# Kernel optimization log

Hardware: AMD Instinct MI355X
Metric: run time of the kernel (lower is better)

Reference implementation:

```python
import jax, jax.numpy as jnp
import numpy as np

SEQ, B, XD = 2048, 4, 16
D, NH, DFF, L, M = 256, 8, 512, 2, 1024
DH = D // NH
NEG_INF = -1e9  # finite stand-in for -inf (same softmax result, grad-safe)


def setup_inputs() -> dict:
    key = jax.random.key(0)
    ks = iter(jax.random.split(key, 40))

    def w(shape, s=0.02):
        return jax.random.normal(next(ks), shape, dtype=jnp.float32) * s

    return {
        "x": jax.random.normal(next(ks), (SEQ, B, XD), dtype=jnp.float32),
        "y": jax.random.normal(next(ks), (SEQ, B), dtype=jnp.float32),
        "single_eval_pos": M,
        "xenc_w": w((D, XD)), "xenc_b": w((D,)),
        "yenc_w": w((D, 1)), "yenc_b": w((D,)),
        "in_proj_w": w((L, 3 * D, D)), "in_proj_b": w((L, 3 * D)),
        "out_proj_w": w((L, D, D)), "out_proj_b": w((L, D)),
        "ln1_g": jnp.ones((L, D), jnp.float32), "ln1_b": jnp.zeros((L, D), jnp.float32),
        "lin1_w": w((L, DFF, D)), "lin1_b": w((L, DFF)),
        "lin2_w": w((L, D, DFF)), "lin2_b": w((L, D)),
        "ln2_g": jnp.ones((L, D), jnp.float32), "ln2_b": jnp.zeros((L, D), jnp.float32),
        "head_w1": w((DFF, D)), "head_b1": w((DFF,)),
        "head_w2": w((1, DFF)), "head_b2": w((1,)),
    }


def _layer_norm(x, g, b, eps=1e-5):
    mu = jnp.mean(x, axis=-1, keepdims=True)
    var = jnp.var(x, axis=-1, keepdims=True)
    return (x - mu) * jax.lax.rsqrt(var + eps) * g + b


def _forward(x, y, M_, p):
    seq, batch = y.shape
    x_src = x @ p["xenc_w"].T + p["xenc_b"]                     # [seq, b, D]
    y_src = y[..., None] @ p["yenc_w"].T + p["yenc_b"]           # [seq, b, D]
    tokens = jnp.concatenate([x_src[:M_] + y_src[:M_], x_src[M_:]], axis=0)

    # prefix-block + diagonal mask: keep (j < M) or (i == j)
    i = jnp.arange(seq)
    keep = (i[None, :] < M_) | (i[:, None] == i[None, :])
    mask = jnp.where(keep, 0.0, NEG_INF).astype(tokens.dtype)    # [seq, seq]

    h = tokens
    for l in range(p["in_proj_w"].shape[0]):
        qkv = h @ p["in_proj_w"][l].T + p["in_proj_b"][l]        # [seq, b, 3D]
        q, k, v = jnp.split(qkv, 3, axis=-1)
        to_heads = lambda t: t.reshape(seq, batch, NH, DH).transpose(1, 2, 0, 3)
        q, k, v = to_heads(q), to_heads(k), to_heads(v)          # [b, h, s, dh]
        scores = jnp.einsum("bhqd,bhkd->bhqk", q, k) / np.float32(np.sqrt(DH)) + mask
        attn = jax.nn.softmax(scores, axis=-1)
        o = jnp.einsum("bhqk,bhkd->bhqd", attn, v)
        o = o.transpose(2, 0, 1, 3).reshape(seq, batch, D)
        o = o @ p["out_proj_w"][l].T + p["out_proj_b"][l]
        h = _layer_norm(h + o, p["ln1_g"][l], p["ln1_b"][l])      # post-norm
        ff = jax.nn.gelu(h @ p["lin1_w"][l].T + p["lin1_b"][l], approximate=False)
        ff = ff @ p["lin2_w"][l].T + p["lin2_b"][l]
        h = _layer_norm(h + ff, p["ln2_g"][l], p["ln2_b"][l])

    q_out = h[M_:]                                               # [seq-M, b, D]
    hid = jax.nn.gelu(q_out @ p["head_w1"].T + p["head_b1"], approximate=False)
    return hid @ p["head_w2"].T + p["head_b2"]                   # [seq-M, b, 1]


def reference(x, y, single_eval_pos, xenc_w, xenc_b, yenc_w, yenc_b,
              in_proj_w, in_proj_b, out_proj_w, out_proj_b,
              ln1_g, ln1_b, lin1_w, lin1_b, lin2_w, lin2_b, ln2_g, ln2_b,
              head_w1, head_b1, head_w2, head_b2):
    p = dict(xenc_w=xenc_w, xenc_b=xenc_b, yenc_w=yenc_w, yenc_b=yenc_b,
             in_proj_w=in_proj_w, in_proj_b=in_proj_b,
             out_proj_w=out_proj_w, out_proj_b=out_proj_b,
             ln1_g=ln1_g, ln1_b=ln1_b, lin1_w=lin1_w, lin1_b=lin1_b,
             lin2_w=lin2_w, lin2_b=lin2_b, ln2_g=ln2_g, ln2_b=ln2_b,
             head_w1=head_w1, head_b1=head_b1, head_w2=head_w2, head_b2=head_b2)
    return _forward(x, y, int(single_eval_pos), p)
```

## Files before the change

### kernel.cpp

```cpp
#include <hip/hip_runtime.h>
#include <hip/hip_bf16.h>
#include <math.h>

#define SEQ    2048
#define BATCH  4
#define XDIM   16
#define DMODEL 256
#define NHEAD  8
#define DH     32
#define DFF    512
#define NLAYER 2
#define MPOS   1024
#define ROWS   (SEQ*BATCH)

#define ATT_SCALE 0.17677669529663687f

typedef __attribute__((ext_vector_type(8))) short bf16x8;
typedef __attribute__((ext_vector_type(4))) float f32x4;

__device__ __forceinline__ float gelu_exact(float x) {
    return 0.5f * x * (1.0f + erff(x * 0.70710678118654752f));
}
__device__ __forceinline__ short f2bf(float f) {
    unsigned int u = __float_as_uint(f);
    u += 0x7FFFu + ((u >> 16) & 1u);
    return (short)(u >> 16);
}
__device__ __forceinline__ float bf2f(unsigned short u) {
    return __uint_as_float(((unsigned int)u) << 16);
}
__device__ __forceinline__ void gload16(const unsigned short* g, unsigned short* l) {
    __builtin_amdgcn_global_load_lds(
        (const __attribute__((address_space(1))) unsigned int*)g,
        (__attribute__((address_space(3))) unsigned int*)l, 16, 0, 0);
}
#define VMWAIT(N) asm volatile("s_waitcnt vmcnt(" #N ")" ::: "memory")
__device__ __forceinline__ void pipe_barrier() {
    __builtin_amdgcn_sched_barrier(0);
    __builtin_amdgcn_s_barrier();
    __builtin_amdgcn_sched_barrier(0);
}

__global__ __launch_bounds__(256) void encode_cast(
    const float* __restrict__ x, const float* __restrict__ y,
    const float* __restrict__ xw, const float* __restrict__ xb,
    const float* __restrict__ yw, const float* __restrict__ yb,
    float* __restrict__ h, unsigned short* __restrict__ hb,
    const float* __restrict__ s0, const float* __restrict__ s1,
    const float* __restrict__ s2, const float* __restrict__ s3,
    const float* __restrict__ s4,
    unsigned short* __restrict__ d0, unsigned short* __restrict__ d1,
    unsigned short* __restrict__ d2, unsigned short* __restrict__ d3,
    unsigned short* __restrict__ d4)
{
    if (blockIdx.x < ROWS/4) {
        int g = blockIdx.x;
        int d = threadIdx.x;
        __shared__ float xs[4][XDIM];
        __shared__ float ys[4];
        if (d < 64) xs[d>>4][d&15] = x[(size_t)(g*4 + (d>>4))*XDIM + (d&15)];
        if (d < 4)  ys[d] = y[g*4 + d];
        __syncthreads();
        float wreg[XDIM];
        #pragma unroll
        for (int k = 0; k < XDIM; ++k) wreg[k] = xw[d*XDIM + k];
        const float xbv = xb[d], ywv = yw[d], ybv = yb[d];
        const bool train = (g < MPOS);
        #pragma unroll
        for (int r = 0; r < 4; ++r) {
            int row = g*4 + r;
            float acc = xbv;
            #pragma unroll
            for (int k = 0; k < XDIM; ++k) acc = fmaf(xs[r][k], wreg[k], acc);
            if (train) acc += ys[r]*ywv + ybv;
            h[(size_t)row*DMODEL + d]  = acc;
            hb[(size_t)row*DMODEL + d] = (unsigned short)f2bf(acc);
        }
        return;
    }
    int i = (blockIdx.x - ROWS/4)*256 + threadIdx.x;
    if (i >= 147456) return;
    const float* s; unsigned short* d; int off;
    if      (i <  49152) { s = s0; d = d0; off = i; }
    else if (i <  65536) { s = s1; d = d1; off = i - 49152; }
    else if (i <  98304) { s = s2; d = d2; off = i - 65536; }
    else if (i < 131072) { s = s3; d = d3; off = i - 98304; }
    else                 { s = s4; d = d4; off = i - 131072; }
    float4 a = *(const float4*)(s + (size_t)off*8);
    float4 c = *(const float4*)(s + (size_t)off*8 + 4);
    ushort4 u0, u1;
    u0.x=(unsigned short)f2bf(a.x); u0.y=(unsigned short)f2bf(a.y);
    u0.z=(unsigned short)f2bf(a.z); u0.w=(unsigned short)f2bf(a.w);
    u1.x=(unsigned short)f2bf(c.x); u1.y=(unsigned short)f2bf(c.y);
    u1.z=(unsigned short)f2bf(c.z); u1.w=(unsigned short)f2bf(c.w);
    *(ushort4*)(d + (size_t)off*8)     = u0;
    *(ushort4*)(d + (size_t)off*8 + 4) = u1;
}

__global__ __launch_bounds__(256) void gemm_qkv(
    const unsigned short* __restrict__ A, const unsigned short* __restrict__ B,
    const float* __restrict__ bias,
    unsigned short* __restrict__ Qg, unsigned short* __restrict__ Kg,
    unsigned short* __restrict__ Vg, int K)
{
    __shared__ unsigned short As[2][128][64];
    __shared__ unsigned short Bs[2][64][64];
    int tid  = threadIdx.x;
    int w    = tid >> 6, lane = tid & 63;
    int col  = lane & 15, quad = lane >> 4;
    int u    = blockIdx.x >> 3, xcd = blockIdx.x & 7;
    int by   = xcd*8 + u/12, bx = u%12;
    int m0   = by * 128, n0 = bx * 64;
    int l8   = lane >> 3;
    int c8s  = (((lane & 7) ^ l8) * 8);

    f32x4 acc[2][4];
    #pragma unroll
    for (int i = 0; i < 2; ++i)
        #pragma unroll
        for (int j = 0; j < 4; ++j) acc[i][j] = (f32x4){0.f,0.f,0.f,0.f};

    const unsigned short* ga = A + (size_t)(m0 + w*32 + l8)*K + c8s;
    const unsigned short* gb = B + (size_t)(n0 + w*16 + l8)*K + c8s;
    const int NS = K / 64;

    #pragma unroll
    for (int t = 0; t < 4; ++t) gload16(ga + (size_t)(t*8)*K, &As[0][w*32 + t*8][0]);
    #pragma unroll
    for (int t = 0; t < 2; ++t) gload16(gb + (size_t)(t*8)*K, &Bs[0][w*16 + t*8][0]);

    for (int s = 0; s < NS; ++s) {
        VMWAIT(0);
        pipe_barrier();
        if (s + 1 < NS) {
            int k2 = (s + 1) * 64;
            int nb = (s + 1) & 1;
            #pragma unroll
            for (int t = 0; t < 4; ++t) gload16(ga + k2 + (size_t)(t*8)*K, &As[nb][w*32 + t*8][0]);
            #pragma unroll
            for (int t = 0; t < 2; ++t) gload16(gb + k2 + (size_t)(t*8)*K, &Bs[nb][w*16 + t*8][0]);
        }
        int cur = s & 1;
        #pragma unroll
        for (int kk = 0; kk < 2; ++kk) {
            const int so = (((kk*4 + quad) ^ (col & 7)) * 8);
            bf16x8 af[2], bfr[4];
            #pragma unroll
            for (int i = 0; i < 2; ++i) af[i]  = *(const bf16x8*)&As[cur][w*32 + i*16 + col][so];
            #pragma unroll
            for (int j = 0; j < 4; ++j) bfr[j] = *(const bf16x8*)&Bs[cur][j*16 + col][so];
            #pragma unroll
            for (int i = 0; i < 2; ++i)
                #pragma unroll
                for (int j = 0; j < 4; ++j)
                    acc[i][j] = __builtin_amdgcn_mfma_f32_16x16x32_bf16(bfr[j], af[i], acc[i][j], 0, 0, 0);
        }
    }

    int region = n0 >> 8;
    if (region < 2) {
        #pragma unroll
        for (int i = 0; i < 2; ++i) {
            int m = m0 + w*32 + i*16 + col;
            int s = m >> 2, bidx = m & 3;
            #pragma unroll
            for (int j = 0; j < 4; ++j) {
                int ng = n0 + j*16 + quad*4;
                float4 bi = *(const float4*)&bias[ng];
                ushort4 uu;
                uu.x=(unsigned short)f2bf(acc[i][j][0] + bi.x);
                uu.y=(unsigned short)f2bf(acc[i][j][1] + bi.y);
                uu.z=(unsigned short)f2bf(acc[i][j][2] + bi.z);
                uu.w=(unsigned short)f2bf(acc[i][j][3] + bi.w);
                int np = ng - (region << 8);
                int hh = np >> 5, d = np & 31;
                int bh = bidx*NHEAD + hh;
                if (region == 0)
                    *(ushort4*)(Qg + ((size_t)(bh*SEQ + s))*DH + d) = uu;
                else
                    *(ushort4*)(Kg + ((size_t)(bh*SEQ + s))*DH + d) = uu;
            }
        }
    } else {
        __syncthreads();
        unsigned short* T3 = (unsigned short*)As;
        #pragma unroll
        for (int i = 0; i < 2; ++i) {
            int mi = w*32 + i*16 + col;
            int ss = mi >> 2, bidx = mi & 3;
            #pragma unroll
            for (int j = 0; j < 4; ++j) {
                int ni = j*16 + quad*4;
                float4 bi = *(const float4*)&bias[n0 + ni];
                T3[((ni    )*4 + bidx)*32 + ss] = (unsigned short)f2bf(acc[i][j][0] + bi.x);
                T3[((ni + 1)*4 + bidx)*32 + ss] = (unsigned short)f2bf(acc[i][j][1] + bi.y);
                T3[((ni + 2)*4 + bidx)*32 + ss] = (unsigned short)f2bf(acc[i][j][2] + bi.z);
                T3[((ni + 3)*4 + bidx)*32 + ss] = (unsigned short)f2bf(acc[i][j][3] + bi.w);
            }
        }
        __syncthreads();
        int sBase = m0 >> 2;
        #pragma unroll
        for (int r = 0; r < 4; ++r) {
            int chunk = tid + 256*r;
            int l = chunk >> 2, p = chunk & 3;
            int d = l & 31, hh_l = (l >> 5) & 1, bidx = l >> 6;
            int ni = hh_l*32 + d;
            int hh = ((n0 & 255) + ni) >> 5;
            int bh = bidx*NHEAD + hh;
            uint4 val = *(const uint4*)&T3[(ni*4 + bidx)*32 + p*8];
            *(uint4*)(Vg + ((size_t)(bh*DH + d))*SEQ + sBase + p*8) = val;
        }
    }
}

__global__ __launch_bounds__(256) void attn_mfma(
    const unsigned short* __restrict__ Qg,
    const unsigned short* __restrict__ Kg,
    const unsigned short* __restrict__ Vg,
    unsigned short* __restrict__ o)
{
    const int id  = blockIdx.x;
    const int sl  = id >> 3;
    const int bh  = (id & 7) * 4 + (sl >> 4);
    const int qt2 = sl & 15;
    const int h   = bh & 7;
    const int b   = bh >> 3;
    const int q0A = qt2 * 64;
    const int q0B = MPOS + qt2 * 64;
    const int tid  = threadIdx.x;
    const int w    = tid >> 6;
    const int lane = tid & 63;
    const int col  = lane & 15;
    const int quad = lane >> 4;

    __shared__ unsigned short Kt[2][128][40];
    __shared__ unsigned short Vt[2][32][136];
    __shared__ unsigned short PtA[4][16][136];
    __shared__ unsigned short PtB[4][16][136];

    const int qA = q0A + 16*w + col;
    const int qB = q0B + 16*w + col;
    bf16x8 qfA = *(const bf16x8*)(Qg + ((size_t)(bh*SEQ + qA))*DH + quad*8);
    bf16x8 qfB = *(const bf16x8*)(Qg + ((size_t)(bh*SEQ + qB))*DH + quad*8);

    f32x4 O0A = {0.f,0.f,0.f,0.f}, O1A = {0.f,0.f,0.f,0.f};
    f32x4 O0B = {0.f,0.f,0.f,0.f}, O1B = {0.f,0.f,0.f,0.f};
    float lsumA = 0.f, lsumB = 0.f;

    const int kRow = tid >> 2, kCh = (tid & 3) * 8;
    const int vD   = tid >> 3, vCh = (tid & 7) * 8;

    uint4 kreg0 = *(const uint4*)(Kg + ((size_t)(bh*SEQ + kRow     ))*DH + kCh);
    uint4 kreg1 = *(const uint4*)(Kg + ((size_t)(bh*SEQ + kRow + 64))*DH + kCh);
    uint4 vreg0 = *(const uint4*)(Vg + ((size_t)(bh*DH + vD))*SEQ + vCh);
    uint4 vreg1 = *(const uint4*)(Vg + ((size_t)(bh*DH + vD))*SEQ + vCh + 64);

    for (int kt = 0; kt < 8; ++kt) {
        const int p = kt & 1;
        *(uint4*)&Kt[p][kRow     ][kCh] = kreg0;
        *(uint4*)&Kt[p][kRow + 64][kCh] = kreg1;
        *(uint4*)&Vt[p][vD][vCh     ]   = vreg0;
        *(uint4*)&Vt[p][vD][vCh + 64]   = vreg1;
        __syncthreads();
        if (kt < 7) {
            int kn = (kt + 1) * 128;
            kreg0 = *(const uint4*)(Kg + ((size_t)(bh*SEQ + kn + kRow     ))*DH + kCh);
            kreg1 = *(const uint4*)(Kg + ((size_t)(bh*SEQ + kn + kRow + 64))*DH + kCh);
            vreg0 = *(const uint4*)(Vg + ((size_t)(bh*DH + vD))*SEQ + kn + vCh);
            vreg1 = *(const uint4*)(Vg + ((size_t)(bh*DH + vD))*SEQ + kn + vCh + 64);
        } else {
            kreg0 = *(const uint4*)(Kg + ((size_t)(bh*SEQ + q0B + kRow))*DH + kCh);
            vreg0 = *(const uint4*)(Vg + ((size_t)(bh*DH + vD))*SEQ + q0B + vCh);
        }

        #pragma unroll
        for (int mt = 0; mt < 8; ++mt) {
            bf16x8 kf = *(const bf16x8*)&Kt[p][mt*16 + col][quad*8];
            f32x4 stA = {0.f,0.f,0.f,0.f};
            stA = __builtin_amdgcn_mfma_f32_16x16x32_bf16(kf, qfA, stA, 0, 0, 0);
            ushort4 pwA;
            #pragma unroll
            for (int i = 0; i < 4; ++i) {
                float pv = __expf(stA[i]*ATT_SCALE);
                unsigned short us = (unsigned short)f2bf(pv);
                ((unsigned short*)&pwA)[i] = us;
                lsumA += bf2f(us);
            }
            *(ushort4*)&PtA[w][col][mt*16 + quad*4] = pwA;

            f32x4 stB = {0.f,0.f,0.f,0.f};
            stB = __builtin_amdgcn_mfma_f32_16x16x32_bf16(kf, qfB, stB, 0, 0, 0);
            ushort4 pwB;
            #pragma unroll
            for (int i = 0; i < 4; ++i) {
                float pv = __expf(stB[i]*ATT_SCALE);
                unsigned short us = (unsigned short)f2bf(pv);
                ((unsigned short*)&pwB)[i] = us;
                lsumB += bf2f(us);
            }
            *(ushort4*)&PtB[w][col][mt*16 + quad*4] = pwB;
        }
        #pragma unroll
        for (int c = 0; c < 4; ++c) {
            bf16x8 v0 = *(const bf16x8*)&Vt[p][col     ][c*32 + quad*8];
            bf16x8 v1 = *(const bf16x8*)&Vt[p][col + 16][c*32 + quad*8];
            bf16x8 pfA = *(const bf16x8*)&PtA[w][col][c*32 + quad*8];
            O0A = __builtin_amdgcn_mfma_f32_16x16x32_bf16(v0, pfA, O0A, 0, 0, 0);
            O1A = __builtin_amdgcn_mfma_f32_16x16x32_bf16(v1, pfA, O1A, 0, 0, 0);
            bf16x8 pfB = *(const bf16x8*)&PtB[w][col][c*32 + quad*8];
            O0B = __builtin_amdgcn_mfma_f32_16x16x32_bf16(v0, pfB, O0B, 0, 0, 0);
            O1B = __builtin_amdgcn_mfma_f32_16x16x32_bf16(v1, pfB, O1B, 0, 0, 0);
        }
    }

    *(uint4*)&Kt[0][kRow][kCh] = kreg0;
    *(uint4*)&Vt[0][vD][vCh]   = vreg0;
    __syncthreads();
    #pragma unroll
    for (int mt = 0; mt < 4; ++mt) {
        bf16x8 kf = *(const bf16x8*)&Kt[0][mt*16 + col][quad*8];
        f32x4 stB = {0.f,0.f,0.f,0.f};
        stB = __builtin_amdgcn_mfma_f32_16x16x32_bf16(kf, qfB, stB, 0, 0, 0);
        ushort4 pwB;
        #pragma unroll
        for (int i = 0; i < 4; ++i) {
            float pv = __expf(stB[i]*ATT_SCALE);
            if (mt*16 + quad*4 + i != 16*w + col) pv = 0.f;
            unsigned short us = (unsigned short)f2bf(pv);
            ((unsigned short*)&pwB)[i] = us;
            lsumB += bf2f(us);
        }
        *(ushort4*)&PtB[w][col][mt*16 + quad*4] = pwB;
    }
    #pragma unroll
    for (int c = 0; c < 2; ++c) {
        bf16x8 v0 = *(const bf16x8*)&Vt[0][col     ][c*32 + quad*8];
        bf16x8 v1 = *(const bf16x8*)&Vt[0][col + 16][c*32 + quad*8];
        bf16x8 pfB = *(const bf16x8*)&PtB[w][col][c*32 + quad*8];
        O0B = __builtin_amdgcn_mfma_f32_16x16x32_bf16(v0, pfB, O0B, 0, 0, 0);
        O1B = __builtin_amdgcn_mfma_f32_16x16x32_bf16(v1, pfB, O1B, 0, 0, 0);
    }

    lsumA += __shfl_xor(lsumA, 16, 64); lsumA += __shfl_xor(lsumA, 32, 64);
    lsumB += __shfl_xor(lsumB, 16, 64); lsumB += __shfl_xor(lsumB, 32, 64);
    float invA = 1.0f / lsumA, invB = 1.0f / lsumB;
    ushort4 u0, u1;
    #pragma unroll
    for (int i = 0; i < 4; ++i) {
        ((unsigned short*)&u0)[i] = (unsigned short)f2bf(O0A[i]*invA);
        ((unsigned short*)&u1)[i] = (unsigned short)f2bf(O1A[i]*invA);
    }
    unsigned short* opA = o + ((size_t)(qA*BATCH + b))*DMODEL + h*DH;
    *(ushort4*)(opA + quad*4)      = u0;
    *(ushort4*)(opA + 16 + quad*4) = u1;
    #pragma unroll
    for (int i = 0; i < 4; ++i) {
        ((unsigned short*)&u0)[i] = (unsigned short)f2bf(O0B[i]*invB);
        ((unsigned short*)&u1)[i] = (unsigned short)f2bf(O1B[i]*invB);
    }
    unsigned short* opB = o + ((size_t)(qB*BATCH + b))*DMODEL + h*DH;
    *(ushort4*)(opB + quad*4)      = u0;
    *(ushort4*)(opB + 16 + quad*4) = u1;
}

__global__ __launch_bounds__(512) void mlp_fused(
    const unsigned short* __restrict__ attb,
    const unsigned short* __restrict__ Wout, const float* __restrict__ ob,
    const float* __restrict__ g1, const float* __restrict__ be1,
    const unsigned short* __restrict__ W1, const float* __restrict__ fb1,
    const unsigned short* __restrict__ W2, const float* __restrict__ fb2,
    const float* __restrict__ g2, const float* __restrict__ be2,
    float* __restrict__ h, unsigned short* __restrict__ hb,
    const unsigned short* __restrict__ Wh1, const float* __restrict__ hb1,
    const float* __restrict__ hw2, const float* __restrict__ hb2,
    float* __restrict__ out, int doHead)
{
    __shared__ unsigned short Bs[3][256][64];
    __shared__ __align__(16) unsigned char smem_u[33280];
    __shared__ unsigned short Ht[2][16][264];
    __shared__ float sP[2][8][16], qP[2][8][16];

    typedef unsigned short AsT[2][16][64];
    AsT* As = reinterpret_cast<AsT*>(smem_u);
    typedef unsigned short PtT[16][520];
    PtT* Pt = reinterpret_cast<PtT*>(smem_u);

    const int tid  = threadIdx.x;
    const int w    = tid >> 6;
    const int lane = tid & 63;
    const int col  = lane & 15;
    const int quad = lane >> 4;
    const int l8   = lane >> 3;
    const int c8s  = (((lane & 7) ^ l8) * 8);
    const int bid  = blockIdx.x;
    const int m0a  = bid * 16;
    const int m0b  = 4096 + bid * 16;
    const int ma   = m0a + col;
    const int mb   = m0b + col;

    float resid[2][2][4];

    {
        f32x4 acc[2][2];
        #pragma unroll
        for (int g = 0; g < 2; ++g)
            #pragma unroll
            for (int j = 0; j < 2; ++j) acc[g][j] = (f32x4){0.f,0.f,0.f,0.f};

        const int gr = w >> 1;
        const unsigned short* gaw = attb + (size_t)((gr ? m0b : m0a) + (w&1)*8 + l8)*DMODEL + c8s;
        const unsigned short* gb  = Wout + (size_t)(w*32 + l8)*DMODEL + c8s;
        const int NS = DMODEL / 64;

        #pragma unroll
        for (int pb = 0; pb < 2; ++pb) {
            int k = pb * 64;
            if (w < 4) gload16(gaw + k, &As[pb][gr][(w&1)*8][0]);
            #pragma unroll
            for (int t = 0; t < 4; ++t)
                gload16(gb + k + (size_t)(t*8)*DMODEL, &Bs[pb][w*32 + t*8][0]);
        }
        int bcur = 0;
        for (int s = 0; s < NS; ++s) {
            if (s == NS - 1)      { VMWAIT(0); }
            else if (w < 4)       { VMWAIT(5); }
            else                  { VMWAIT(4); }
            pipe_barrier();
            if (s + 2 < NS) {
                int bpre = bcur + 2; if (bpre >= 3) bpre -= 3;
                int k2 = (s + 2) * 64;
                if (w < 4) gload16(gaw + k2, &As[bpre][gr][(w&1)*8][0]);
                #pragma unroll
                for (int t = 0; t < 4; ++t)
                    gload16(gb + k2 + (size_t)(t*8)*DMODEL, &Bs[bpre][w*32 + t*8][0]);
            }
            #pragma unroll
            for (int kk = 0; kk < 2; ++kk) {
                const int so = (((kk*4 + quad) ^ (col & 7)) * 8);
                bf16x8 af0 = *(const bf16x8*)&As[bcur][0][col][so];
                bf16x8 af1 = *(const bf16x8*)&As[bcur][1][col][so];
                #pragma unroll
                for (int j = 0; j < 2; ++j) {
                    bf16x8 bfr = *(const bf16x8*)&Bs[bcur][w*32 + j*16 + col][so];
                    acc[0][j] = __builtin_amdgcn_mfma_f32_16x16x32_bf16(bfr, af0, acc[0][j], 0, 0, 0);
                    acc[1][j] = __builtin_amdgcn_mfma_f32_16x16x32_bf16(bfr, af1, acc[1][j], 0, 0, 0);
                }
            }
            bcur = (bcur == 2) ? 0 : bcur + 1;
        }

        float ssum[2] = {0.f, 0.f}, qsum[2] = {0.f, 0.f};
        #pragma unroll
        for (int g = 0; g < 2; ++g) {
            int m = g ? mb : ma;
            #pragma unroll
            for (int j = 0; j < 2; ++j) {
                int n = w*32 + j*16 + quad*4;
                float4 bi = *(const float4*)&ob[n];
                float4 hv = *(const float4*)&h[(size_t)m*DMODEL + n];
                #pragma unroll
                for (int i = 0; i < 4; ++i) {
                    float val = acc[g][j][i] + ((const float*)&bi)[i] + ((const float*)&hv)[i];
                    resid[g][j][i] = val;
                    ssum[g] += val; qsum[g] += val*val;
                }
            }
        }
        #pragma unroll
        for (int g = 0; g < 2; ++g) {
            ssum[g] += __shfl_xor(ssum[g], 16, 64); ssum[g] += __shfl_xor(ssum[g], 32, 64);
            qsum[g] += __shfl_xor(qsum[g], 16, 64); qsum[g] += __shfl_xor(qsum[g], 32, 64);
        }
        if (quad == 0) {
            sP[0][w][col] = ssum[0]; qP[0][w][col] = qsum[0];
            sP[1][w][col] = ssum[1]; qP[1][w][col] = qsum[1];
        }
        __syncthreads();
        #pragma unroll
        for (int g = 0; g < 2; ++g) {
            float st = 0.f, qt = 0.f;
            #pragma unroll
            for (int ww = 0; ww < 8; ++ww) { st += sP[g][ww][col]; qt += qP[g][ww][col]; }
            float mu   = st * (1.0f/DMODEL);
            float var  = qt * (1.0f/DMODEL) - mu*mu;
            float rstd = rsqrtf(var + 1e-5f);
            #pragma unroll
            for (int j = 0; j < 2; ++j) {
                int n = w*32 + j*16 + quad*4;
                float4 gv = *(const float4*)&g1[n];
                float4 bv = *(const float4*)&be1[n];
                ushort4 u;
                #pragma unroll
                for (int i = 0; i < 4; ++i) {
                    float o = (resid[g][j][i]-mu)*rstd*((const float*)&gv)[i] + ((const float*)&bv)[i];
                    resid[g][j][i] = o;
                    ((unsigned short*)&u)[i] = (unsigned short)f2bf(o);
                }
                *(ushort4*)&Ht[g][col][n] = u;
            }
        }
        __syncthreads();
    }

    #pragma unroll 1
    for (int nh = 0; nh < 2; ++nh) {
        f32x4 acc[2][2];
        #pragma unroll
        for (int g = 0; g < 2; ++g)
            #pragma unroll
            for (int j = 0; j < 2; ++j) acc[g][j] = (f32x4){0.f,0.f,0.f,0.f};
        const unsigned short* gb = W1 + (size_t)(nh*256 + w*32 + l8)*DMODEL + c8s;
        const int NS = DMODEL / 64;

        #pragma unroll
        for (int pb = 0; pb < 2; ++pb)
            #pragma unroll
            for (int t = 0; t < 4; ++t)
                gload16(gb + pb*64 + (size_t)(t*8)*DMODEL, &Bs[pb][w*32 + t*8][0]);

        int bcur = 0;
        for (int s = 0; s < NS; ++s) {
            if (s == NS - 1) { VMWAIT(0); } else { VMWAIT(4); }
            pipe_barrier();
            if (s + 2 < NS) {
                int bpre = bcur + 2; if (bpre >= 3) bpre -= 3;
                int k2 = (s + 2) * 64;
                #pragma unroll
                for (int t = 0; t < 4; ++t)
                    gload16(gb + k2 + (size_t)(t*8)*DMODEL, &Bs[bpre][w*32 + t*8][0]);
            }
            #pragma unroll
            for (int kk = 0; kk < 2; ++kk) {
                const int so = (((kk*4 + quad) ^ (col & 7)) * 8);
                bf16x8 af0 = *(const bf16x8*)&Ht[0][col][s*64 + kk*32 + quad*8];
                bf16x8 af1 = *(const bf16x8*)&Ht[1][col][s*64 + kk*32 + quad*8];
                #pragma unroll
                for (int j = 0; j < 2; ++j) {
                    bf16x8 bfr = *(const bf16x8*)&Bs[bcur][w*32 + j*16 + col][so];
                    acc[0][j] = __builtin_amdgcn_mfma_f32_16x16x32_bf16(bfr, af0, acc[0][j], 0, 0, 0);
                    acc[1][j] = __builtin_amdgcn_mfma_f32_16x16x32_bf16(bfr, af1, acc[1][j], 0, 0, 0);
                }
            }
            bcur = (bcur == 2) ? 0 : bcur + 1;
        }
        #pragma unroll
        for (int g = 0; g < 2; ++g)
            #pragma unroll
            for (int j = 0; j < 2; ++j) {
                int n2 = nh*256 + w*32 + j*16 + quad*4;
                float4 bi = *(const float4*)&fb1[n2];
                ushort4 u;
                #pragma unroll
                for (int i = 0; i < 4; ++i)
                    ((unsigned short*)&u)[i] = (unsigned short)f2bf(gelu_exact(acc[g][j][i] + ((const float*)&bi)[i]));
                *(ushort4*)&Pt[g][col][n2] = u;
            }
        pipe_barrier();
    }

    {
        __syncthreads();
        f32x4 acc[2][2];
        #pragma unroll
        for (int g = 0; g < 2; ++g)
            #pragma unroll
            for (int j = 0; j < 2; ++j) acc[g][j] = (f32x4){0.f,0.f,0.f,0.f};
        const unsigned short* gb = W2 + (size_t)(w*32 + l8)*DFF + c8s;
        const int NS = DFF / 64;

        #pragma unroll
        for (int pb = 0; pb < 2; ++pb)
            #pragma unroll
            for (int t = 0; t < 4; ++t)
                gload16(gb + pb*64 + (size_t)(t*8)*DFF, &Bs[pb][w*32 + t*8][0]);

        int bcur = 0;
        for (int s = 0; s < NS; ++s) {
            if (s == NS - 1) { VMWAIT(0); } else { VMWAIT(4); }
            pipe_barrier();
            if (s + 2 < NS) {
                int bpre = bcur + 2; if (bpre >= 3) bpre -= 3;
                int k2 = (s + 2) * 64;
                #pragma unroll
                for (int t = 0; t < 4; ++t)
                    gload16(gb + k2 + (size_t)(t*8)*DFF, &Bs[bpre][w*32 + t*8][0]);
            }
            #pragma unroll
            for (int kk = 0; kk < 2; ++kk) {
                const int so = (((kk*4 + quad) ^ (col & 7)) * 8);
                bf16x8 af0 = *(const bf16x8*)&Pt[0][col][s*64 + kk*32 + quad*8];
                bf16x8 af1 = *(const bf16x8*)&Pt[1][col][s*64 + kk*32 + quad*8];
                #pragma unroll
                for (int j = 0; j < 2; ++j) {
                    bf16x8 bfr = *(const bf16x8*)&Bs[bcur][w*32 + j*16 + col][so];
                    acc[0][j] = __builtin_amdgcn_mfma_f32_16x16x32_bf16(bfr, af0, acc[0][j], 0, 0, 0);
                    acc[1][j] = __builtin_amdgcn_mfma_f32_16x16x32_bf16(bfr, af1, acc[1][j], 0, 0, 0);
                }
            }
            bcur = (bcur == 2) ? 0 : bcur + 1;
        }

        float ssum[2] = {0.f, 0.f}, qsum[2] = {0.f, 0.f};
        #pragma unroll
        for (int g = 0; g < 2; ++g)
            #pragma unroll
            for (int j = 0; j < 2; ++j) {
                int n = w*32 + j*16 + quad*4;
                float4 bi = *(const float4*)&fb2[n];
                #pragma unroll
                for (int i = 0; i < 4; ++i) {
                    float val = acc[g][j][i] + ((const float*)&bi)[i] + resid[g][j][i];
                    resid[g][j][i] = val;
                    ssum[g] += val; qsum[g] += val*val;
                }
            }
        #pragma unroll
        for (int g = 0; g < 2; ++g) {
            ssum[g] += __shfl_xor(ssum[g], 16, 64); ssum[g] += __shfl_xor(ssum[g], 32, 64);
            qsum[g] += __shfl_xor(qsum[g], 16, 64); qsum[g] += __shfl_xor(qsum[g], 32, 64);
        }
        if (quad == 0) {
            sP[0][w][col] = ssum[0]; qP[0][w][col] = qsum[0];
            sP[1][w][col] = ssum[1]; qP[1][w][col] = qsum[1];
        }
        __syncthreads();
        #pragma unroll
        for (int g = 0; g < 2; ++g) {
            int m = g ? mb : ma;
            float st = 0.f, qt = 0.f;
            #pragma unroll
            for (int ww = 0; ww < 8; ++ww) { st += sP[g][ww][col]; qt += qP[g][ww][col]; }
            float mu   = st * (1.0f/DMODEL);
            float var  = qt * (1.0f/DMODEL) - mu*mu;
            float rstd = rsqrtf(var + 1e-5f);
            #pragma unroll
            for (int j = 0; j < 2; ++j) {
                int n = w*32 + j*16 + quad*4;
                float4 gv = *(const float4*)&g2[n];
                float4 bv = *(const float4*)&be2[n];
                float4 o;
                ushort4 u;
                #pragma unroll
                for (int i = 0; i < 4; ++i) {
                    float ov = (resid[g][j][i]-mu)*rstd*((const float*)&gv)[i] + ((const float*)&bv)[i];
                    ((float*)&o)[i] = ov;
                    ((unsigned short*)&u)[i] = (unsigned short)f2bf(ov);
                }
                *(float4*)&h[(size_t)m*DMODEL + n] = o;
                *(ushort4*)(hb + (size_t)m*DMODEL + n) = u;
                *(ushort4*)&Ht[g][col][n] = u;
            }
        }
        __syncthreads();
    }

    if (doHead) {
        float sdot = 0.f;
        #pragma unroll 1
        for (int nh = 0; nh < 2; ++nh) {
            f32x4 acc[2];
            #pragma unroll
            for (int j = 0; j < 2; ++j) acc[j] = (f32x4){0.f,0.f,0.f,0.f};
            const unsigned short* gb = Wh1 + (size_t)(nh*256 + w*32 + l8)*DMODEL + c8s;
            const int NS = DMODEL / 64;

            #pragma unroll
            for (int pb = 0; pb < 2; ++pb)
                #pragma unroll
                for (int t = 0; t < 4; ++t)
                    gload16(gb + pb*64 + (size_t)(t*8)*DMODEL, &Bs[pb][w*32 + t*8][0]);

            int bcur = 0;
            for (int s = 0; s < NS; ++s) {
                if (s == NS - 1) { VMWAIT(0); } else { VMWAIT(4); }
                pipe_barrier();
                if (s + 2 < NS) {
                    int bpre = bcur + 2; if (bpre >= 3) bpre -= 3;
                    int k2 = (s + 2) * 64;
                    #pragma unroll
                    for (int t = 0; t < 4; ++t)
                        gload16(gb + k2 + (size_t)(t*8)*DMODEL, &Bs[bpre][w*32 + t*8][0]);
                }
                #pragma unroll
                for (int kk = 0; kk < 2; ++kk) {
                    const int so = (((kk*4 + quad) ^ (col & 7)) * 8);
                    bf16x8 af = *(const bf16x8*)&Ht[1][col][s*64 + kk*32 + quad*8];
                    #pragma unroll
                    for (int j = 0; j < 2; ++j) {
                        bf16x8 bfr = *(const bf16x8*)&Bs[bcur][w*32 + j*16 + col][so];
                        acc[j] = __builtin_amdgcn_mfma_f32_16x16x32_bf16(bfr, af, acc[j], 0, 0, 0);
                    }
                }
                bcur = (bcur == 2) ? 0 : bcur + 1;
            }
            #pragma unroll
            for (int j = 0; j < 2; ++j) {
                int n2 = nh*256 + w*32 + j*16 + quad*4;
                float4 b1v = *(const float4*)&hb1[n2];
                float4 w2v = *(const float4*)&hw2[n2];
                #pragma unroll
                for (int i = 0; i < 4; ++i)
                    sdot += gelu_exact(acc[j][i] + ((const float*)&b1v)[i]) * ((const float*)&w2v)[i];
            }
            pipe_barrier();
        }
        sdot += __shfl_xor(sdot, 16, 64); sdot += __shfl_xor(sdot, 32, 64);
        if (quad == 0) sP[0][w][col] = sdot;
        __syncthreads();
        if (tid < 16) {
            float r = hb2[0];
            #pragma unroll
            for (int ww = 0; ww < 8; ++ww) r += sP[0][ww][tid];
            out[bid*16 + tid] = r;
        }
    }
}

extern "C" void kernel_launch(void* const* d_in, const int* in_sizes, int n_in,
                              void* d_out, int out_size, void* d_ws, size_t ws_size,
                              hipStream_t stream)
{
    const float* x        = (const float*)d_in[0];
    const float* y        = (const float*)d_in[1];
    const float* xenc_w   = (const float*)d_in[3];
    const float* xenc_b   = (const float*)d_in[4];
    const float* yenc_w   = (const float*)d_in[5];
    const float* yenc_b   = (const float*)d_in[6];
    const float* in_proj_w  = (const float*)d_in[7];
    const float* in_proj_b  = (const float*)d_in[8];
    const float* out_proj_w = (const float*)d_in[9];
    const float* out_proj_b = (const float*)d_in[10];
    const float* ln1_g    = (const float*)d_in[11];
    const float* ln1_b    = (const float*)d_in[12];
    const float* lin1_w   = (const float*)d_in[13];
    const float* lin1_b   = (const float*)d_in[14];
    const float* lin2_w   = (const float*)d_in[15];
    const float* lin2_b   = (const float*)d_in[16];
    const float* ln2_g    = (const float*)d_in[17];
    const float* ln2_b    = (const float*)d_in[18];
    const float* head_w1  = (const float*)d_in[19];
    const float* head_b1  = (const float*)d_in[20];
    const float* head_w2  = (const float*)d_in[21];
    const float* head_b2  = (const float*)d_in[22];
    float* out = (float*)d_out;

    float* ws  = (float*)d_ws;
    float* h    = ws;
    unsigned short* hb    = (unsigned short*)(h + (size_t)ROWS*DMODEL);
    unsigned short* attb  = hb    + (size_t)ROWS*DMODEL;
    unsigned short* Qg    = attb  + (size_t)ROWS*DMODEL;
    unsigned short* Kg    = Qg    + (size_t)BATCH*NHEAD*SEQ*DH;
    unsigned short* Vg    = Kg    + (size_t)BATCH*NHEAD*SEQ*DH;
    unsigned short* Wqkv  = Vg    + (size_t)BATCH*NHEAD*SEQ*DH;
    unsigned short* Wout  = Wqkv  + (size_t)NLAYER*3*DMODEL*DMODEL;
    unsigned short* Wl1   = Wout  + (size_t)NLAYER*DMODEL*DMODEL;
    unsigned short* Wl2   = Wl1   + (size_t)NLAYER*DFF*DMODEL;
    unsigned short* Wh1   = Wl2   + (size_t)NLAYER*DMODEL*DFF;

    encode_cast<<<ROWS/4 + 576, 256, 0, stream>>>(
        x, y, xenc_w, xenc_b, yenc_w, yenc_b, h, hb,
        in_proj_w, out_proj_w, lin1_w, lin2_w, head_w1,
        Wqkv, Wout, Wl1, Wl2, Wh1);

    for (int l = 0; l < NLAYER; ++l) {
        gemm_qkv<<<768, 256, 0, stream>>>(
            hb, Wqkv + (size_t)l*3*DMODEL*DMODEL, in_proj_b + l*3*DMODEL,
            Qg, Kg, Vg, DMODEL);
        attn_mfma<<<512, 256, 0, stream>>>(Qg, Kg, Vg, attb);
        mlp_fused<<<256, 512, 0, stream>>>(
            attb,
            Wout + (size_t)l*DMODEL*DMODEL, out_proj_b + l*DMODEL,
            ln1_g + l*DMODEL, ln1_b + l*DMODEL,
            Wl1 + (size_t)l*DFF*DMODEL, lin1_b + l*DFF,
            Wl2 + (size_t)l*DMODEL*DFF, lin2_b + l*DMODEL,
            ln2_g + l*DMODEL, ln2_b + l*DMODEL,
            h, hb,
            Wh1, head_b1, head_w2, head_b2,
            out, (l == NLAYER-1) ? 1 : 0);
    }
}
```

Before: 229.9 us.

## Split attention query groups across 8 waves instead of 4 per block

The attention kernel now launches 512 threads per block. Waves 0-3 handle the context query tile and waves 4-7 handle the matching test query tile, where before each of 4 waves processed both tiles. Each thread loads one K and one V chunk instead of two, and the tail diagonal step runs only in the second group. This halves per-wave register and serial MFMA/exp work and adds more waves for latency hiding. In exchange there are more threads per sync and the first group sits idle during the tail step.

Result: no change. 226.3 us (-1.6%).

```diff
diff --git a/kernel.cpp b/kernel.cpp
--- a/kernel.cpp
+++ b/kernel.cpp
@@ -214,7 +214,7 @@
     }
 }
 
-__global__ __launch_bounds__(256) void attn_mfma(
+__global__ __launch_bounds__(512) void attn_mfma(
     const unsigned short* __restrict__ Qg,
     const unsigned short* __restrict__ Kg,
     const unsigned short* __restrict__ Vg,
@@ -230,138 +230,113 @@
     const int q0B = MPOS + qt2 * 64;
     const int tid  = threadIdx.x;
     const int w    = tid >> 6;
+    const int ws   = w & 3;
+    const int grp  = w >> 2;
     const int lane = tid & 63;
     const int col  = lane & 15;
     const int quad = lane >> 4;
 
     __shared__ unsigned short Kt[2][128][40];
     __shared__ unsigned short Vt[2][32][136];
-    __shared__ unsigned short PtA[4][16][136];
-    __shared__ unsigned short PtB[4][16][136];
-
-    const int qA = q0A + 16*w + col;
-    const int qB = q0B + 16*w + col;
-    bf16x8 qfA = *(const bf16x8*)(Qg + ((size_t)(bh*SEQ + qA))*DH + quad*8);
-    bf16x8 qfB = *(const bf16x8*)(Qg + ((size_t)(bh*SEQ + qB))*DH + quad*8);
-
-    f32x4 O0A = {0.f,0.f,0.f,0.f}, O1A = {0.f,0.f,0.f,0.f};
-    f32x4 O0B = {0.f,0.f,0.f,0.f}, O1B = {0.f,0.f,0.f,0.f};
-    float lsumA = 0.f, lsumB = 0.f;
-
-    const int kRow = tid >> 2, kCh = (tid & 3) * 8;
-    const int vD   = tid >> 3, vCh = (tid & 7) * 8;
-
-    uint4 kreg0 = *(const uint4*)(Kg + ((size_t)(bh*SEQ + kRow     ))*DH + kCh);
-    uint4 kreg1 = *(const uint4*)(Kg + ((size_t)(bh*SEQ + kRow + 64))*DH + kCh);
-    uint4 vreg0 = *(const uint4*)(Vg + ((size_t)(bh*DH + vD))*SEQ + vCh);
-    uint4 vreg1 = *(const uint4*)(Vg + ((size_t)(bh*DH + vD))*SEQ + vCh + 64);
+    __shared__ unsigned short Pt[8][16][136];
+
+    const int q0 = grp ? q0B : q0A;
+    const int q  = q0 + 16*ws + col;
+    bf16x8 qf = *(const bf16x8*)(Qg + ((size_t)(bh*SEQ + q))*DH + quad*8);
+
+    f32x4 O0 = {0.f,0.f,0.f,0.f};
+    f32x4 O1 = {0.f,0.f,0.f,0.f};
+    float lsum = 0.f;
+
+    const int kRow = tid >> 2,  kCh = (tid & 3) * 8;
+    const int vD   = tid >> 4,  vCh = (tid & 15) * 8;
+
+    uint4 kreg = *(const uint4*)(Kg + ((size_t)(bh*SEQ + kRow))*DH + kCh);
+    uint4 vreg = *(const uint4*)(Vg + ((size_t)(bh*DH + vD))*SEQ + vCh);
 
     for (int kt = 0; kt < 8; ++kt) {
         const int p = kt & 1;
-        *(uint4*)&Kt[p][kRow     ][kCh] = kreg0;
-        *(uint4*)&Kt[p][kRow + 64][kCh] = kreg1;
-        *(uint4*)&Vt[p][vD][vCh     ]   = vreg0;
-        *(uint4*)&Vt[p][vD][vCh + 64]   = vreg1;
+        *(uint4*)&Kt[p][kRow][kCh] = kreg;
+        *(uint4*)&Vt[p][vD][vCh]   = vreg;
         __syncthreads();
         if (kt < 7) {
             int kn = (kt + 1) * 128;
-            kreg0 = *(const uint4*)(Kg + ((size_t)(bh*SEQ + kn + kRow     ))*DH + kCh);
-            kreg1 = *(const uint4*)(Kg + ((size_t)(bh*SEQ + kn + kRow + 64))*DH + kCh);
-            vreg0 = *(const uint4*)(Vg + ((size_t)(bh*DH + vD))*SEQ + kn + vCh);
-            vreg1 = *(const uint4*)(Vg + ((size_t)(bh*DH + vD))*SEQ + kn + vCh + 64);
+            kreg = *(const uint4*)(Kg + ((size_t)(bh*SEQ + kn + kRow))*DH + kCh);
+            vreg = *(const uint4*)(Vg + ((size_t)(bh*DH + vD))*SEQ + kn + vCh);
         } else {
-            kreg0 = *(const uint4*)(Kg + ((size_t)(bh*SEQ + q0B + kRow))*DH + kCh);
-            vreg0 = *(const uint4*)(Vg + ((size_t)(bh*DH + vD))*SEQ + q0B + vCh);
+            if (kRow < 64)
+                kreg = *(const uint4*)(Kg + ((size_t)(bh*SEQ + q0B + kRow))*DH + kCh);
+            if (vCh < 64)
+                vreg = *(const uint4*)(Vg + ((size_t)(bh*DH + vD))*SEQ + q0B + vCh);
         }
 
         #pragma unroll
         for (int mt = 0; mt < 8; ++mt) {
             bf16x8 kf = *(const bf16x8*)&Kt[p][mt*16 + col][quad*8];
-            f32x4 stA = {0.f,0.f,0.f,0.f};
-            stA = __builtin_amdgcn_mfma_f32_16x16x32_bf16(kf, qfA, stA, 0, 0, 0);
-            ushort4 pwA;
+            f32x4 st = {0.f,0.f,0.f,0.f};
+            st = __builtin_amdgcn_mfma_f32_16x16x32_bf16(kf, qf, st, 0, 0, 0);
+            ushort4 pw;
             #pragma unroll
             for (int i = 0; i < 4; ++i) {
-                float pv = __expf(stA[i]*ATT_SCALE);
+                float pv = __expf(st[i]*ATT_SCALE);
                 unsigned short us = (unsigned short)f2bf(pv);
-                ((unsigned short*)&pwA)[i] = us;
-                lsumA += bf2f(us);
-            }
-            *(ushort4*)&PtA[w][col][mt*16 + quad*4] = pwA;
-
-            f32x4 stB = {0.f,0.f,0.f,0.f};
-            stB = __builtin_amdgcn_mfma_f32_16x16x32_bf16(kf, qfB, stB, 0, 0, 0);
-            ushort4 pwB;
-            #pragma unroll
-            for (int i = 0; i < 4; ++i) {
-                float pv = __expf(stB[i]*ATT_SCALE);
-                unsigned short us = (unsigned short)f2bf(pv);
-                ((unsigned short*)&pwB)[i] = us;
-                lsumB += bf2f(us);
-            }
-            *(ushort4*)&PtB[w][col][mt*16 + quad*4] = pwB;
+                ((unsigned short*)&pw)[i] = us;
+                lsum += bf2f(us);
+            }
+            *(ushort4*)&Pt[w][col][mt*16 + quad*4] = pw;
         }
         #pragma unroll
         for (int c = 0; c < 4; ++c) {
             bf16x8 v0 = *(const bf16x8*)&Vt[p][col     ][c*32 + quad*8];
             bf16x8 v1 = *(const bf16x8*)&Vt[p][col + 16][c*32 + quad*8];
-            bf16x8 pfA = *(const bf16x8*)&PtA[w][col][c*32 + quad*8];
-            O0A = __builtin_amdgcn_mfma_f32_16x16x32_bf16(v0, pfA, O0A, 0, 0, 0);
-            O1A = __builtin_amdgcn_mfma_f32_16x16x32_bf16(v1, pfA, O1A, 0, 0, 0);
-            bf16x8 pfB = *(const bf16x8*)&PtB[w][col][c*32 + quad*8];
-            O0B = __builtin_amdgcn_mfma_f32_16x16x32_bf16(v0, pfB, O0B, 0, 0, 0);
-            O1B = __builtin_amdgcn_mfma_f32_16x16x32_bf16(v1, pfB, O1B, 0, 0, 0);
-        }
-    }
-
-    *(uint4*)&Kt[0][kRow][kCh] = kreg0;
-    *(uint4*)&Vt[0][vD][vCh]   = vreg0;
+            bf16x8 pf = *(const bf16x8*)&Pt[w][col][c*32 + quad*8];
+            O0 = __builtin_amdgcn_mfma_f32_16x16x32_bf16(v0, pf, O0, 0, 0, 0);
+            O1 = __builtin_amdgcn_mfma_f32_16x16x32_bf16(v1, pf, O1, 0, 0, 0);
+        }
+    }
+
+    if (kRow < 64) *(uint4*)&Kt[0][kRow][kCh] = kreg;
+    if (vCh < 64)  *(uint4*)&Vt[0][vD][vCh]   = vreg;
     __syncthreads();
-    #pragma unroll
-    for (int mt = 0; mt < 4; ++mt) {
-        bf16x8 kf = *(const bf16x8*)&Kt[0][mt*16 + col][quad*8];
-        f32x4 stB = {0.f,0.f,0.f,0.f};
-        stB = __builtin_amdgcn_mfma_f32_16x16x32_bf16(kf, qfB, stB, 0, 0, 0);
-        ushort4 pwB;
-        #pragma unroll
-        for (int i = 0; i < 4; ++i) {
-            float pv = __expf(stB[i]*ATT_SCALE);
-            if (mt*16 + quad*4 + i != 16*w + col) pv = 0.f;
-            unsigned short us = (unsigned short)f2bf(pv);
-            ((unsigned short*)&pwB)[i] = us;
-            lsumB += bf2f(us);
-        }
-        *(ushort4*)&PtB[w][col][mt*16 + quad*4] = pwB;
-    }
-    #pragma unroll
-    for (int c = 0; c < 2; ++c) {
-        bf16x8 v0 = *(const bf16x8*)&Vt[0][col     ][c*32 + quad*8];
-        bf16x8 v1 = *(const bf16x8*)&Vt[0][col + 16][c*32 + quad*8];
-        bf16x8 pfB = *(const bf16x8*)&PtB[w][col][c*32 + quad*8];
-        O0B = __builtin_amdgcn_mfma_f32_16x16x32_bf16(v0, pfB, O0B, 0, 0, 0);
-        O1B = __builtin_amdgcn_mfma_f32_16x16x32_bf16(v1, pfB, O1B, 0, 0, 0);
-    }
-
-    lsumA += __shfl_xor(lsumA, 16, 64); lsumA += __shfl_xor(lsumA, 32, 64);
-    lsumB += __shfl_xor(lsumB, 16, 64); lsumB += __shfl_xor(lsumB, 32, 64);
-    float invA = 1.0f / lsumA, invB = 1.0f / lsumB;
+    if (grp == 1) {
+        #pragma unroll
+        for (int mt = 0; mt < 4; ++mt) {
+            bf16x8 kf = *(const bf16x8*)&Kt[0][mt*16 + col][quad*8];
+            f32x4 st = {0.f,0.f,0.f,0.f};
+            st = __builtin_amdgcn_mfma_f32_16x16x32_bf16(kf, qf, st, 0, 0, 0);
+            ushort4 pw;
+            #pragma unroll
+            for (int i = 0; i < 4; ++i) {
+                float pv = __expf(st[i]*ATT_SCALE);
+                if (mt*16 + quad*4 + i != 16*ws + col) pv = 0.f;
+                unsigned short us = (unsigned short)f2bf(pv);
+                ((unsigned short*)&pw)[i] = us;
+                lsum += bf2f(us);
+            }
+            *(ushort4*)&Pt[w][col][mt*16 + quad*4] = pw;
+        }
+        #pragma unroll
+        for (int c = 0; c < 2; ++c) {
+            bf16x8 v0 = *(const bf16x8*)&Vt[0][col     ][c*32 + quad*8];
+            bf16x8 v1 = *(const bf16x8*)&Vt[0][col + 16][c*32 + quad*8];
+            bf16x8 pf = *(const bf16x8*)&Pt[w][col][c*32 + quad*8];
+            O0 = __builtin_amdgcn_mfma_f32_16x16x32_bf16(v0, pf, O0, 0, 0, 0);
+            O1 = __builtin_amdgcn_mfma_f32_16x16x32_bf16(v1, pf, O1, 0, 0, 0);
+        }
+    }
+
+    lsum += __shfl_xor(lsum, 16, 64);
+    lsum += __shfl_xor(lsum, 32, 64);
+    float inv = 1.0f / lsum;
     ushort4 u0, u1;
     #pragma unroll
     for (int i = 0; i < 4; ++i) {
-        ((unsigned short*)&u0)[i] = (unsigned short)f2bf(O0A[i]*invA);
-        ((unsigned short*)&u1)[i] = (unsigned short)f2bf(O1A[i]*invA);
-    }
-    unsigned short* opA = o + ((size_t)(qA*BATCH + b))*DMODEL + h*DH;
-    *(ushort4*)(opA + quad*4)      = u0;
-    *(ushort4*)(opA + 16 + quad*4) = u1;
-    #pragma unroll
-    for (int i = 0; i < 4; ++i) {
-        ((unsigned short*)&u0)[i] = (unsigned short)f2bf(O0B[i]*invB);
-        ((unsigned short*)&u1)[i] = (unsigned short)f2bf(O1B[i]*invB);
-    }
-    unsigned short* opB = o + ((size_t)(qB*BATCH + b))*DMODEL + h*DH;
-    *(ushort4*)(opB + quad*4)      = u0;
-    *(ushort4*)(opB + 16 + quad*4) = u1;
+        ((unsigned short*)&u0)[i] = (unsigned short)f2bf(O0[i]*inv);
+        ((unsigned short*)&u1)[i] = (unsigned short)f2bf(O1[i]*inv);
+    }
+    unsigned short* op = o + ((size_t)(q*BATCH + b))*DMODEL + h*DH;
+    *(ushort4*)(op + quad*4)      = u0;
+    *(ushort4*)(op + 16 + quad*4) = u1;
 }
 
 __global__ __launch_bounds__(512) void mlp_fused(
@@ -767,7 +742,7 @@
         gemm_qkv<<<768, 256, 0, stream>>>(
             hb, Wqkv + (size_t)l*3*DMODEL*DMODEL, in_proj_b + l*3*DMODEL,
             Qg, Kg, Vg, DMODEL);
-        attn_mfma<<<512, 256, 0, stream>>>(Qg, Kg, Vg, attb);
+        attn_mfma<<<512, 512, 0, stream>>>(Qg, Kg, Vg, attb);
         mlp_fused<<<256, 512, 0, stream>>>(
             attb,
             Wout + (size_t)l*DMODEL*DMODEL, out_proj_b + l*DMODEL,
```
